# Performance work log

Hardware: AMD Instinct MI355X
Metric: run time of the kernel (lower is better)

## Reference

```python
import jax, jax.numpy as jnp
import numpy as np

DMODEL = 1024
DHIDDEN = 1024
N_HEAD = 16
HEAD_DIM = DHIDDEN // N_HEAD
B, S = 4, 2048


def setup_inputs() -> dict:
    key = jax.random.key(0)
    ks = jax.random.split(key, 10)
    sc = 1.0 / np.sqrt(DMODEL)
    return {
        "x": jax.random.normal(ks[0], (B, S, DMODEL), dtype=jnp.float32),
        "Wq": jax.random.normal(ks[1], (DMODEL, DHIDDEN), dtype=jnp.float32) * sc,
        "bq": jnp.zeros((DHIDDEN,), dtype=jnp.float32),
        "Wk": jax.random.normal(ks[2], (DMODEL, DHIDDEN), dtype=jnp.float32) * sc,
        "bk": jnp.zeros((DHIDDEN,), dtype=jnp.float32),
        "Wv": jax.random.normal(ks[3], (DMODEL, DHIDDEN), dtype=jnp.float32) * sc,
        "bv": jnp.zeros((DHIDDEN,), dtype=jnp.float32),
        "Wo": jax.random.normal(ks[4], (DHIDDEN, DMODEL), dtype=jnp.float32) * sc,
        "bo": jnp.zeros((DMODEL,), dtype=jnp.float32),
        "ln_gamma": jnp.ones((DMODEL,), dtype=jnp.float32),
        "ln_beta": jnp.zeros((DMODEL,), dtype=jnp.float32),
    }


def _layernorm(x, gamma, beta, eps=1e-5):
    mu = jnp.mean(x, axis=-1, keepdims=True)
    var = jnp.var(x, axis=-1, keepdims=True)
    return (x - mu) * jax.lax.rsqrt(var + eps) * gamma + beta


def reference(x, Wq, bq, Wk, bk, Wv, bv, Wo, bo, ln_gamma, ln_beta):
    b, s, _ = x.shape
    h = _layernorm(x, ln_gamma, ln_beta)           # [B,S,D]
    q = h @ Wq + bq                                 # [B,S,Dh]
    k = h @ Wk + bk
    v = h @ Wv + bv
    # [B,H,S,hd]
    q = q.reshape(b, s, N_HEAD, HEAD_DIM).transpose(0, 2, 1, 3)
    k = k.reshape(b, s, N_HEAD, HEAD_DIM).transpose(0, 2, 1, 3)
    v = v.reshape(b, s, N_HEAD, HEAD_DIM).transpose(0, 2, 1, 3)
    scores = jnp.einsum("bhqd,bhkd->bhqk", q, k) / np.sqrt(HEAD_DIM)
    causal = jnp.tril(jnp.ones((s, s), dtype=bool))  # [S,S]
    scores = jnp.where(causal, scores, jnp.finfo(scores.dtype).min)
    attn = jax.nn.softmax(scores, axis=-1)           # [B,H,S,S]
    out = jnp.einsum("bhqk,bhkd->bhqd", attn, v)     # [B,H,S,hd]
    out = out.transpose(0, 2, 1, 3).reshape(b, s, DHIDDEN)
    return out @ Wo + bo
```

## Files before the change

### kernel.cpp

```cpp
#include <hip/hip_runtime.h>


typedef short short8 __attribute__((ext_vector_type(8)));
typedef float floatx4 __attribute__((ext_vector_type(4)));
typedef unsigned short ushort4v __attribute__((ext_vector_type(4)));
typedef unsigned int uint2v __attribute__((ext_vector_type(2)));

#define MFMA16(a, b, c) __builtin_amdgcn_mfma_f32_16x16x32_bf16((a), (b), (c), 0, 0, 0)

__device__ __forceinline__ unsigned short f2bf(float f) {
  unsigned int u = __float_as_uint(f);
  u += 0x7FFFu + ((u >> 16) & 1u);
  return (unsigned short)(u >> 16);
}

#if defined(__has_builtin)
#if __has_builtin(__builtin_amdgcn_cvt_pk_bf16_f32)
#define HAVE_PK_BF16 1
#endif
#endif

__device__ __forceinline__ unsigned int pk_bf16(float a, float b) {
#ifdef HAVE_PK_BF16
  typedef __bf16 bf16x2_t __attribute__((ext_vector_type(2)));
  union { bf16x2_t v; unsigned int u; } cvt;
  cvt.v = __builtin_amdgcn_cvt_pk_bf16_f32(a, b);
  return cvt.u;
#else
  return (unsigned int)f2bf(a) | ((unsigned int)f2bf(b) << 16);
#endif
}

__device__ __forceinline__ void async_lds16(const void* g, void* l) {
  __builtin_amdgcn_global_load_lds(
      (const __attribute__((address_space(1))) void*)g,
      (__attribute__((address_space(3))) void*)l, 16, 0, 0);
}

__global__ __launch_bounds__(256) void transpose_w(
    const float* __restrict__ wq, const float* __restrict__ wk,
    const float* __restrict__ wv, const float* __restrict__ wo,
    unsigned short* __restrict__ wqkvT, unsigned short* __restrict__ woT) {
  __shared__ float t[64][65];
  const int r = threadIdx.x >> 6, c = threadIdx.x & 63;
  const int n0 = blockIdx.x * 64, k0 = blockIdx.y * 64, mz = blockIdx.z;
  const float* src = (mz == 0) ? wq : (mz == 1) ? wk : (mz == 2) ? wv : wo;
  unsigned short* dst = (mz == 3) ? woT : (wqkvT + (size_t)mz * 1024 * 1024);
#pragma unroll
  for (int i = r; i < 64; i += 4) t[i][c] = src[(size_t)(k0 + i) * 1024 + n0 + c];
  __syncthreads();
#pragma unroll
  for (int i = r; i < 64; i += 4) dst[(size_t)(n0 + i) * 1024 + k0 + c] = f2bf(t[c][i]);
}

__global__ __launch_bounds__(256) void ln_kernel(
    const float* __restrict__ x, const float* __restrict__ gamma,
    const float* __restrict__ beta, unsigned short* __restrict__ h) {
  const int row = blockIdx.x, tid = threadIdx.x;
  const float4 xv = ((const float4*)(x + (size_t)row * 1024))[tid];
  float s = xv.x + xv.y + xv.z + xv.w;
  float q = xv.x * xv.x + xv.y * xv.y + xv.z * xv.z + xv.w * xv.w;
#pragma unroll
  for (int off = 32; off > 0; off >>= 1) {
    s += __shfl_xor(s, off, 64);
    q += __shfl_xor(q, off, 64);
  }
  __shared__ float sm[4], qm[4];
  const int wave = tid >> 6, lane = tid & 63;
  if (lane == 0) { sm[wave] = s; qm[wave] = q; }
  __syncthreads();
  s = sm[0] + sm[1] + sm[2] + sm[3];
  q = qm[0] + qm[1] + qm[2] + qm[3];
  const float mean = s * (1.0f / 1024.0f);
  const float var = q * (1.0f / 1024.0f) - mean * mean;
  const float rstd = rsqrtf(var + 1e-5f);
  const float4 g = ((const float4*)gamma)[tid];
  const float4 bb = ((const float4*)beta)[tid];
  ushort4v o;
  o.x = f2bf((xv.x - mean) * rstd * g.x + bb.x);
  o.y = f2bf((xv.y - mean) * rstd * g.y + bb.y);
  o.z = f2bf((xv.z - mean) * rstd * g.z + bb.z);
  o.w = f2bf((xv.w - mean) * rstd * g.w + bb.w);
  ((ushort4v*)(h + (size_t)row * 1024))[tid] = o;
}

#define GEMM128_MAIN(A_, Bt_)                                                   \
  __shared__ __align__(16) unsigned short lA[128 * 32];                         \
  __shared__ __align__(16) unsigned short lB[128 * 32];                         \
  const int tid = threadIdx.x;                                                  \
  const int wave = tid >> 6, lane = tid & 63, quad = lane >> 4, l15 = lane & 15;\
  const int wm = wave >> 1, wn = wave & 1;                                      \
  const int m0 = blockIdx.x * 128, n0 = blockIdx.y * 128;                       \
  const int srow = tid >> 2, schunk = tid & 3;                                  \
  floatx4 acc[4][4];                                                            \
  _Pragma("unroll") for (int i = 0; i < 4; i++)                                 \
  _Pragma("unroll") for (int j = 0; j < 4; j++)                                 \
      acc[i][j] = (floatx4){0.f, 0.f, 0.f, 0.f};                                \
  for (int kt = 0; kt < 32; kt++) {                                             \
    const int k0 = kt * 32;                                                     \
    __syncthreads();                                                            \
    _Pragma("unroll") for (int j = 0; j < 2; j++) {                             \
      async_lds16(A_ + (size_t)(m0 + j * 64 + srow) * 1024 + k0 + schunk * 8,   \
                  (char*)lA + j * 4096 + wave * 1024);                          \
      async_lds16(Bt_ + (size_t)(n0 + j * 64 + srow) * 1024 + k0 + schunk * 8,  \
                  (char*)lB + j * 4096 + wave * 1024);                          \
    }                                                                           \
    __syncthreads();                                                            \
    short8 af[4], bf[4];                                                        \
    _Pragma("unroll") for (int i = 0; i < 4; i++) {                             \
      af[i] = *(const short8*)(lA + (wm * 64 + i * 16 + l15) * 32 + quad * 8);  \
      bf[i] = *(const short8*)(lB + (wn * 64 + i * 16 + l15) * 32 + quad * 8);  \
    }                                                                           \
    _Pragma("unroll") for (int mt = 0; mt < 4; mt++)                            \
    _Pragma("unroll") for (int nt = 0; nt < 4; nt++)                            \
        acc[mt][nt] = MFMA16(af[mt], bf[nt], acc[mt][nt]);                      \
  }

__global__ __launch_bounds__(256) void gemm_qkv(
    const unsigned short* __restrict__ A, const unsigned short* __restrict__ Bt,
    const float* __restrict__ bq, const float* __restrict__ bk,
    const float* __restrict__ bv, unsigned short* __restrict__ qo,
    unsigned short* __restrict__ ko, unsigned short* __restrict__ vT) {
  GEMM128_MAIN(A, Bt)
  const int sel = n0 >> 10;
  const float* bias = (sel == 0) ? bq : (sel == 1) ? bk : bv;
  const float oscale = (sel == 0) ? 0.18033688011112042f : 1.0f;
#pragma unroll
  for (int nt = 0; nt < 4; nt++) {
    const int n = n0 + wn * 64 + nt * 16 + l15;
    const int nn = n & 1023;
    const float bia = bias[nn];
    const int hidx = nn >> 6, d = nn & 63;
#pragma unroll
    for (int mt = 0; mt < 4; mt++) {
      const int mb = m0 + wm * 64 + mt * 16 + quad * 4;
      const int b = mb >> 11, sdx = mb & 2047;
      if (sel == 2) {
        ushort4v pk;
#pragma unroll
        for (int r = 0; r < 4; r++) pk[r] = f2bf(acc[mt][nt][r] + bia);
        *(ushort4v*)(vT + ((size_t)(b * 16 + hidx) * 64 + d) * 2048 + sdx) = pk;
      } else {
        unsigned short* dst =
            ((sel == 0) ? qo : ko) + ((size_t)(b * 16 + hidx) * 2048 + sdx) * 64 + d;
#pragma unroll
        for (int r = 0; r < 4; r++)
          dst[(size_t)r * 64] = f2bf((acc[mt][nt][r] + bia) * oscale);
      }
    }
  }
}

__global__ __launch_bounds__(256) void gemm_out(
    const unsigned short* __restrict__ A, const unsigned short* __restrict__ Bt,
    const float* __restrict__ bo, float* __restrict__ out) {
  GEMM128_MAIN(A, Bt)
#pragma unroll
  for (int nt = 0; nt < 4; nt++) {
    const int n = n0 + wn * 64 + nt * 16 + l15;
    const float bia = bo[n];
#pragma unroll
    for (int mt = 0; mt < 4; mt++) {
      const int m = m0 + wm * 64 + mt * 16 + quad * 4;
#pragma unroll
      for (int r = 0; r < 4; r++) out[(size_t)(m + r) * 1024 + n] = acc[mt][nt][r] + bia;
    }
  }
}

__global__ __launch_bounds__(256) void attn_kernel(
    const unsigned short* __restrict__ q, const unsigned short* __restrict__ k,
    const unsigned short* __restrict__ vT, unsigned short* __restrict__ ao) {
  __shared__ __align__(16) unsigned short lK[2][64 * 64];
  __shared__ __align__(16) unsigned short lV[2][64 * 64];
  __shared__ __align__(16) unsigned short lP[4][16 * 64];
  const int tid = threadIdx.x;
  const int wave = tid >> 6, lane = tid & 63, quad = lane >> 4, l15 = lane & 15;
  const int id = (int)blockIdx.x;
  const int bh = (id & 7) * 8 + ((id >> 3) & 7);
  const int qx = id >> 6;
  const int b = bh >> 4, hh = bh & 15;

  const unsigned short* qb = q + (size_t)bh * 2048 * 64;
  const unsigned short* kb = k + (size_t)bh * 2048 * 64;
  const unsigned short* vb = vT + (size_t)bh * 64 * 2048;
  unsigned short* pw = &lP[wave][0];

  const int srow = tid >> 3, schunk = tid & 7;

  const short8 ones8 = {0x3F80, 0x3F80, 0x3F80, 0x3F80,
                        0x3F80, 0x3F80, 0x3F80, 0x3F80};

  const int sw = l15 & 7;
  const int ph0 = (0 * 4 + quad) ^ sw, ph1 = (1 * 4 + quad) ^ sw;

#define STAGE_TILE(src_, rstride_, cbase_, dst_)                                 \
  _Pragma("unroll") for (int j = 0; j < 2; j++) {                                \
    const int row_ = j * 32 + srow;                                              \
    const int gch_ = schunk ^ (row_ & 7);                                        \
    async_lds16(src_ + (size_t)row_ * (rstride_) + (cbase_) + gch_ * 8,          \
                (char*)(dst_) + j * 4096 + wave * 1024);                         \
  }

#pragma unroll 1
  for (int pass = 0; pass < 2; pass++) {
    const int qt = pass ? qx : 31 - qx;
    const int q0w = qt * 64 + wave * 16;
    const int ntiles = qt + 1;

    short8 qf[2];
#pragma unroll
    for (int hf = 0; hf < 2; hf++)
      qf[hf] = *(const short8*)(qb + (size_t)(q0w + l15) * 64 + hf * 32 + quad * 8);

    floatx4 o[4];
#pragma unroll
    for (int nt = 0; nt < 4; nt++) o[nt] = (floatx4){0.f, 0.f, 0.f, 0.f};
    floatx4 lacc = {0.f, 0.f, 0.f, 0.f};

    __syncthreads();
    STAGE_TILE(kb, 64, 0, &lK[0][0])
    STAGE_TILE(vb, 2048, 0, &lV[0][0])
    int kbase = 0;
    for (int t = 0; t < ntiles; t++, kbase += 64) {
      __syncthreads();
      if (t + 1 < ntiles) {
        const int nb = (t + 1) & 1;
        STAGE_TILE(kb, 64, (size_t)(kbase + 64) * 64, &lK[nb][0])
        STAGE_TILE(vb, 2048, kbase + 64, &lV[nb][0])
      }
      const unsigned short* lKc = &lK[t & 1][0];
      const unsigned short* lVc = &lV[t & 1][0];

      floatx4 sc[4];
#pragma unroll
      for (int nt = 0; nt < 4; nt++) {
        sc[nt] = (floatx4){0.f, 0.f, 0.f, 0.f};
        {
          const short8 kf0 = *(const short8*)(lKc + (nt * 16 + l15) * 64 + ph0 * 8);
          sc[nt] = MFMA16(kf0, qf[0], sc[nt]);
          const short8 kf1 = *(const short8*)(lKc + (nt * 16 + l15) * 64 + ph1 * 8);
          sc[nt] = MFMA16(kf1, qf[1], sc[nt]);
        }
      }

      const bool needmask = (kbase + 63 > q0w);
      const int qg = q0w + l15;
#pragma unroll
      for (int nt = 0; nt < 4; nt++) {
        float p0 = exp2f(sc[nt][0]), p1 = exp2f(sc[nt][1]);
        float p2 = exp2f(sc[nt][2]), p3 = exp2f(sc[nt][3]);
        if (needmask) {
          const int kk = kbase + nt * 16 + quad * 4;
          if (kk + 0 > qg) p0 = 0.f;
          if (kk + 1 > qg) p1 = 0.f;
          if (kk + 2 > qg) p2 = 0.f;
          if (kk + 3 > qg) p3 = 0.f;
        }
        uint2v pk2;
        pk2.x = pk_bf16(p0, p1);
        pk2.y = pk_bf16(p2, p3);
        const int phys = (nt * 2 + (quad >> 1)) ^ sw;
        *(uint2v*)(pw + l15 * 64 + phys * 8 + (quad & 1) * 4) = pk2;
      }

      asm volatile("s_waitcnt lgkmcnt(0)" ::: "memory");

#pragma unroll
      for (int hf = 0; hf < 2; hf++) {
        const int ph = hf ? ph1 : ph0;
        const short8 pf = *(const short8*)(pw + l15 * 64 + ph * 8);
        lacc = MFMA16(ones8, pf, lacc);
#pragma unroll
        for (int nt = 0; nt < 4; nt++) {
          const short8 vf = *(const short8*)(lVc + (nt * 16 + l15) * 64 + ph * 8);
          o[nt] = MFMA16(vf, pf, o[nt]);
        }
      }
    }

    const float linv = 1.0f / lacc[0];
    unsigned short* dst = ao + ((size_t)b * 2048 + q0w + l15) * 1024 + hh * 64;
#pragma unroll
    for (int nt = 0; nt < 4; nt++) {
      uint2v pk2;
      pk2.x = pk_bf16(o[nt][0] * linv, o[nt][1] * linv);
      pk2.y = pk_bf16(o[nt][2] * linv, o[nt][3] * linv);
      *(uint2v*)(dst + nt * 16 + quad * 4) = pk2;
    }
  }
#undef STAGE_TILE
}

extern "C" void kernel_launch(void* const* d_in, const int* in_sizes, int n_in,
                              void* d_out, int out_size, void* d_ws, size_t ws_size,
                              hipStream_t stream) {
  const float* x = (const float*)d_in[0];
  const float* Wq = (const float*)d_in[1];
  const float* bq = (const float*)d_in[2];
  const float* Wk = (const float*)d_in[3];
  const float* bk = (const float*)d_in[4];
  const float* Wv = (const float*)d_in[5];
  const float* bv = (const float*)d_in[6];
  const float* Wo = (const float*)d_in[7];
  const float* bo = (const float*)d_in[8];
  const float* gamma = (const float*)d_in[9];
  const float* beta = (const float*)d_in[10];
  float* out = (float*)d_out;

  char* ws = (char*)d_ws;
  unsigned short* wqkvT = (unsigned short*)(ws + 0);
  unsigned short* woT   = (unsigned short*)(ws + 6291456);
  unsigned short* h     = (unsigned short*)(ws + 8388608);
  unsigned short* qb    = (unsigned short*)(ws + 25165824);
  unsigned short* kb    = (unsigned short*)(ws + 41943040);
  unsigned short* vT    = (unsigned short*)(ws + 58720256);
  unsigned short* ao    = (unsigned short*)(ws + 75497472);

  hipLaunchKernelGGL(transpose_w, dim3(16, 16, 4), dim3(256), 0, stream,
                     Wq, Wk, Wv, Wo, wqkvT, woT);
  hipLaunchKernelGGL(ln_kernel, dim3(8192), dim3(256), 0, stream, x, gamma, beta, h);
  hipLaunchKernelGGL(gemm_qkv, dim3(64, 24), dim3(256), 0, stream,
                     h, wqkvT, bq, bk, bv, qb, kb, vT);
  hipLaunchKernelGGL(attn_kernel, dim3(1024), dim3(256), 0, stream, qb, kb, vT, ao);
  hipLaunchKernelGGL(gemm_out, dim3(64, 8), dim3(256), 0, stream, ao, woT, bo, out);
}
```

Measured before the change: 288.7 us.

## Remap GEMM blocks per XCD and load attention V fragments directly from global

Both GEMMs now use a 1D grid whose block index is remapped so that the blocks on each XCD share the same column tiles of the weight matrix, aiming for better per-XCD L2 reuse. In the attention kernel, V tiles are no longer staged through LDS with double buffering. Each lane loads its V MFMA fragments straight from global memory into registers at the start of each tile, which removes the V LDS traffic and frees shared memory. The risk is that these global V loads are no longer overlapped via the async LDS pipeline, which may expose latency and raise register pressure.

```diff
diff --git a/kernel.cpp b/kernel.cpp
--- a/kernel.cpp
+++ b/kernel.cpp
@@ -84,13 +84,13 @@
   ((ushort4v*)(h + (size_t)row * 1024))[tid] = o;
 }
 
-#define GEMM128_MAIN(A_, Bt_)                                                   \
+#define GEMM128_MAIN(A_, Bt_, m0_, n0_)                                         \
   __shared__ __align__(16) unsigned short lA[128 * 32];                         \
   __shared__ __align__(16) unsigned short lB[128 * 32];                         \
   const int tid = threadIdx.x;                                                  \
   const int wave = tid >> 6, lane = tid & 63, quad = lane >> 4, l15 = lane & 15;\
   const int wm = wave >> 1, wn = wave & 1;                                      \
-  const int m0 = blockIdx.x * 128, n0 = blockIdx.y * 128;                       \
+  const int m0 = (m0_), n0 = (n0_);                                             \
   const int srow = tid >> 2, schunk = tid & 3;                                  \
   floatx4 acc[4][4];                                                            \
   _Pragma("unroll") for (int i = 0; i < 4; i++)                                 \
@@ -121,7 +121,9 @@
     const float* __restrict__ bq, const float* __restrict__ bk,
     const float* __restrict__ bv, unsigned short* __restrict__ qo,
     unsigned short* __restrict__ ko, unsigned short* __restrict__ vT) {
-  GEMM128_MAIN(A, Bt)
+  const int id = (int)blockIdx.x;
+  const int xcd = id & 7, rr = id >> 3;
+  GEMM128_MAIN(A, Bt, (rr / 3) * 128, (xcd * 3 + (rr % 3)) * 128)
   const int sel = n0 >> 10;
   const float* bias = (sel == 0) ? bq : (sel == 1) ? bk : bv;
   const float oscale = (sel == 0) ? 0.18033688011112042f : 1.0f;
@@ -154,7 +156,8 @@
 __global__ __launch_bounds__(256) void gemm_out(
     const unsigned short* __restrict__ A, const unsigned short* __restrict__ Bt,
     const float* __restrict__ bo, float* __restrict__ out) {
-  GEMM128_MAIN(A, Bt)
+  const int id = (int)blockIdx.x;
+  GEMM128_MAIN(A, Bt, (id >> 3) * 128, (id & 7) * 128)
 #pragma unroll
   for (int nt = 0; nt < 4; nt++) {
     const int n = n0 + wn * 64 + nt * 16 + l15;
@@ -172,7 +175,6 @@
     const unsigned short* __restrict__ q, const unsigned short* __restrict__ k,
     const unsigned short* __restrict__ vT, unsigned short* __restrict__ ao) {
   __shared__ __align__(16) unsigned short lK[2][64 * 64];
-  __shared__ __align__(16) unsigned short lV[2][64 * 64];
   __shared__ __align__(16) unsigned short lP[4][16 * 64];
   const int tid = threadIdx.x;
   const int wave = tid >> 6, lane = tid & 63, quad = lane >> 4, l15 = lane & 15;
@@ -194,12 +196,12 @@
   const int sw = l15 & 7;
   const int ph0 = (0 * 4 + quad) ^ sw, ph1 = (1 * 4 + quad) ^ sw;
 
-#define STAGE_TILE(src_, rstride_, cbase_, dst_)                                 \
+#define STAGE_K(kbase_, buf_)                                                    \
   _Pragma("unroll") for (int j = 0; j < 2; j++) {                                \
     const int row_ = j * 32 + srow;                                              \
     const int gch_ = schunk ^ (row_ & 7);                                        \
-    async_lds16(src_ + (size_t)row_ * (rstride_) + (cbase_) + gch_ * 8,          \
-                (char*)(dst_) + j * 4096 + wave * 1024);                         \
+    async_lds16(kb + (size_t)((kbase_) + row_) * 64 + (size_t)gch_ * 8,          \
+                (char*)&lK[buf_][0] + j * 4096 + wave * 1024);                   \
   }
 
 #pragma unroll 1
@@ -219,18 +221,21 @@
     floatx4 lacc = {0.f, 0.f, 0.f, 0.f};
 
     __syncthreads();
-    STAGE_TILE(kb, 64, 0, &lK[0][0])
-    STAGE_TILE(vb, 2048, 0, &lV[0][0])
+    STAGE_K(0, 0)
     int kbase = 0;
     for (int t = 0; t < ntiles; t++, kbase += 64) {
       __syncthreads();
-      if (t + 1 < ntiles) {
-        const int nb = (t + 1) & 1;
-        STAGE_TILE(kb, 64, (size_t)(kbase + 64) * 64, &lK[nb][0])
-        STAGE_TILE(vb, 2048, kbase + 64, &lV[nb][0])
-      }
+
+      short8 vf[4][2];
+#pragma unroll
+      for (int nt = 0; nt < 4; nt++)
+#pragma unroll
+        for (int hf = 0; hf < 2; hf++)
+          vf[nt][hf] = *(const short8*)(vb + (size_t)(nt * 16 + l15) * 2048 + kbase +
+                                        hf * 32 + quad * 8);
+
+      if (t + 1 < ntiles) { STAGE_K(kbase + 64, (t + 1) & 1) }
       const unsigned short* lKc = &lK[t & 1][0];
-      const unsigned short* lVc = &lV[t & 1][0];
 
       floatx4 sc[4];
 #pragma unroll
@@ -272,10 +277,7 @@
         const short8 pf = *(const short8*)(pw + l15 * 64 + ph * 8);
         lacc = MFMA16(ones8, pf, lacc);
 #pragma unroll
-        for (int nt = 0; nt < 4; nt++) {
-          const short8 vf = *(const short8*)(lVc + (nt * 16 + l15) * 64 + ph * 8);
-          o[nt] = MFMA16(vf, pf, o[nt]);
-        }
+        for (int nt = 0; nt < 4; nt++) o[nt] = MFMA16(vf[nt][hf], pf, o[nt]);
       }
     }
 
@@ -289,7 +291,7 @@
       *(uint2v*)(dst + nt * 16 + quad * 4) = pk2;
     }
   }
-#undef STAGE_TILE
+#undef STAGE_K
 }
 
 extern "C" void kernel_launch(void* const* d_in, const int* in_sizes, int n_in,
@@ -320,8 +322,8 @@
   hipLaunchKernelGGL(transpose_w, dim3(16, 16, 4), dim3(256), 0, stream,
                      Wq, Wk, Wv, Wo, wqkvT, woT);
   hipLaunchKernelGGL(ln_kernel, dim3(8192), dim3(256), 0, stream, x, gamma, beta, h);
-  hipLaunchKernelGGL(gemm_qkv, dim3(64, 24), dim3(256), 0, stream,
+  hipLaunchKernelGGL(gemm_qkv, dim3(1536), dim3(256), 0, stream,
                      h, wqkvT, bq, bk, bv, qb, kb, vT);
   hipLaunchKernelGGL(attn_kernel, dim3(1024), dim3(256), 0, stream, qb, kb, vT, ao);
-  hipLaunchKernelGGL(gemm_out, dim3(64, 8), dim3(256), 0, stream, ao, woT, bo, out);
-}
+  hipLaunchKernelGGL(gemm_out, dim3(512), dim3(256), 0, stream, ao, woT, bo, out);
+}
```

Measured after the change: 379.4 us. 31.4% more time.

## Fuse attention's two query-tile passes into one K/V sweep and remap GEMM blocks per XCD

Applied to the files above, without the earlier changes.

The attention kernel used to make two sequential passes (query tile 31-qx, then qx), each streaming K/V separately. It now processes both query tiles in one loop over the longer tile's K/V range, sharing each staged K/V tile and its LDS fragment loads across both. It also requests 4 blocks per CU via launch bounds. The QKV and output GEMMs switch to a 1D grid with a block-id remap so each XCD works on a contiguous group of weight columns, aiming for better L2 reuse. The cost is higher register pressure from doubled accumulators, and extra branching on the dual flag.

```diff
diff --git a/kernel.cpp b/kernel.cpp
--- a/kernel.cpp
+++ b/kernel.cpp
@@ -84,13 +84,13 @@
   ((ushort4v*)(h + (size_t)row * 1024))[tid] = o;
 }
 
-#define GEMM128_MAIN(A_, Bt_)                                                   \
+#define GEMM128_MAIN(A_, Bt_, m0_, n0_)                                         \
   __shared__ __align__(16) unsigned short lA[128 * 32];                         \
   __shared__ __align__(16) unsigned short lB[128 * 32];                         \
   const int tid = threadIdx.x;                                                  \
   const int wave = tid >> 6, lane = tid & 63, quad = lane >> 4, l15 = lane & 15;\
   const int wm = wave >> 1, wn = wave & 1;                                      \
-  const int m0 = blockIdx.x * 128, n0 = blockIdx.y * 128;                       \
+  const int m0 = (m0_), n0 = (n0_);                                             \
   const int srow = tid >> 2, schunk = tid & 3;                                  \
   floatx4 acc[4][4];                                                            \
   _Pragma("unroll") for (int i = 0; i < 4; i++)                                 \
@@ -121,7 +121,9 @@
     const float* __restrict__ bq, const float* __restrict__ bk,
     const float* __restrict__ bv, unsigned short* __restrict__ qo,
     unsigned short* __restrict__ ko, unsigned short* __restrict__ vT) {
-  GEMM128_MAIN(A, Bt)
+  const int id = (int)blockIdx.x;
+  const int xcd = id & 7, rr = id >> 3;
+  GEMM128_MAIN(A, Bt, (rr / 3) * 128, (xcd * 3 + (rr % 3)) * 128)
   const int sel = n0 >> 10;
   const float* bias = (sel == 0) ? bq : (sel == 1) ? bk : bv;
   const float oscale = (sel == 0) ? 0.18033688011112042f : 1.0f;
@@ -154,7 +156,8 @@
 __global__ __launch_bounds__(256) void gemm_out(
     const unsigned short* __restrict__ A, const unsigned short* __restrict__ Bt,
     const float* __restrict__ bo, float* __restrict__ out) {
-  GEMM128_MAIN(A, Bt)
+  const int id = (int)blockIdx.x;
+  GEMM128_MAIN(A, Bt, (id >> 3) * 128, (id & 7) * 128)
 #pragma unroll
   for (int nt = 0; nt < 4; nt++) {
     const int n = n0 + wn * 64 + nt * 16 + l15;
@@ -168,7 +171,7 @@
   }
 }
 
-__global__ __launch_bounds__(256) void attn_kernel(
+__global__ __launch_bounds__(256, 4) void attn_kernel(
     const unsigned short* __restrict__ q, const unsigned short* __restrict__ k,
     const unsigned short* __restrict__ vT, unsigned short* __restrict__ ao) {
   __shared__ __align__(16) unsigned short lK[2][64 * 64];
@@ -180,6 +183,9 @@
   const int bh = (id & 7) * 8 + ((id >> 3) & 7);
   const int qx = id >> 6;
   const int b = bh >> 4, hh = bh & 15;
+  const int qtA = 31 - qx, qtB = qx;
+  const int q0wA = qtA * 64 + wave * 16, q0wB = qtB * 64 + wave * 16;
+  const int ntiles = qtA + 1;
 
   const unsigned short* qb = q + (size_t)bh * 2048 * 64;
   const unsigned short* kb = k + (size_t)bh * 2048 * 64;
@@ -202,54 +208,57 @@
                 (char*)(dst_) + j * 4096 + wave * 1024);                         \
   }
 
-#pragma unroll 1
-  for (int pass = 0; pass < 2; pass++) {
-    const int qt = pass ? qx : 31 - qx;
-    const int q0w = qt * 64 + wave * 16;
-    const int ntiles = qt + 1;
-
-    short8 qf[2];
-#pragma unroll
-    for (int hf = 0; hf < 2; hf++)
-      qf[hf] = *(const short8*)(qb + (size_t)(q0w + l15) * 64 + hf * 32 + quad * 8);
-
-    floatx4 o[4];
-#pragma unroll
-    for (int nt = 0; nt < 4; nt++) o[nt] = (floatx4){0.f, 0.f, 0.f, 0.f};
-    floatx4 lacc = {0.f, 0.f, 0.f, 0.f};
-
+  short8 qfA[2], qfB[2];
+#pragma unroll
+  for (int hf = 0; hf < 2; hf++) {
+    qfA[hf] = *(const short8*)(qb + (size_t)(q0wA + l15) * 64 + hf * 32 + quad * 8);
+    qfB[hf] = *(const short8*)(qb + (size_t)(q0wB + l15) * 64 + hf * 32 + quad * 8);
+  }
+
+  floatx4 oA[4], oB[4];
+#pragma unroll
+  for (int nt = 0; nt < 4; nt++) {
+    oA[nt] = (floatx4){0.f, 0.f, 0.f, 0.f};
+    oB[nt] = (floatx4){0.f, 0.f, 0.f, 0.f};
+  }
+  floatx4 laccA = {0.f, 0.f, 0.f, 0.f}, laccB = {0.f, 0.f, 0.f, 0.f};
+
+  STAGE_TILE(kb, 64, 0, &lK[0][0])
+  STAGE_TILE(vb, 2048, 0, &lV[0][0])
+  int kbase = 0;
+  for (int t = 0; t < ntiles; t++, kbase += 64) {
     __syncthreads();
-    STAGE_TILE(kb, 64, 0, &lK[0][0])
-    STAGE_TILE(vb, 2048, 0, &lV[0][0])
-    int kbase = 0;
-    for (int t = 0; t < ntiles; t++, kbase += 64) {
-      __syncthreads();
-      if (t + 1 < ntiles) {
-        const int nb = (t + 1) & 1;
-        STAGE_TILE(kb, 64, (size_t)(kbase + 64) * 64, &lK[nb][0])
-        STAGE_TILE(vb, 2048, kbase + 64, &lV[nb][0])
-      }
-      const unsigned short* lKc = &lK[t & 1][0];
-      const unsigned short* lVc = &lV[t & 1][0];
-
-      floatx4 sc[4];
+    if (t + 1 < ntiles) {
+      const int nb = (t + 1) & 1;
+      STAGE_TILE(kb, 64, (size_t)(kbase + 64) * 64, &lK[nb][0])
+      STAGE_TILE(vb, 2048, (size_t)(kbase + 64), &lV[nb][0])
+    }
+    const unsigned short* lKc = &lK[t & 1][0];
+    const unsigned short* lVc = &lV[t & 1][0];
+    const bool dual = (t <= qtB);
+
+    floatx4 scA[4], scB[4];
+#pragma unroll
+    for (int nt = 0; nt < 4; nt++) {
+      scA[nt] = (floatx4){0.f, 0.f, 0.f, 0.f};
+      scB[nt] = (floatx4){0.f, 0.f, 0.f, 0.f};
+      const short8 kf0 = *(const short8*)(lKc + (nt * 16 + l15) * 64 + ph0 * 8);
+      const short8 kf1 = *(const short8*)(lKc + (nt * 16 + l15) * 64 + ph1 * 8);
+      scA[nt] = MFMA16(kf0, qfA[0], scA[nt]);
+      scA[nt] = MFMA16(kf1, qfA[1], scA[nt]);
+      if (dual) {
+        scB[nt] = MFMA16(kf0, qfB[0], scB[nt]);
+        scB[nt] = MFMA16(kf1, qfB[1], scB[nt]);
+      }
+    }
+
+    {
+      const bool needmask = (kbase + 63 > q0wA);
+      const int qg = q0wA + l15;
 #pragma unroll
       for (int nt = 0; nt < 4; nt++) {
-        sc[nt] = (floatx4){0.f, 0.f, 0.f, 0.f};
-        {
-          const short8 kf0 = *(const short8*)(lKc + (nt * 16 + l15) * 64 + ph0 * 8);
-          sc[nt] = MFMA16(kf0, qf[0], sc[nt]);
-          const short8 kf1 = *(const short8*)(lKc + (nt * 16 + l15) * 64 + ph1 * 8);
-          sc[nt] = MFMA16(kf1, qf[1], sc[nt]);
-        }
-      }
-
-      const bool needmask = (kbase + 63 > q0w);
-      const int qg = q0w + l15;
-#pragma unroll
-      for (int nt = 0; nt < 4; nt++) {
-        float p0 = exp2f(sc[nt][0]), p1 = exp2f(sc[nt][1]);
-        float p2 = exp2f(sc[nt][2]), p3 = exp2f(sc[nt][3]);
+        float p0 = exp2f(scA[nt][0]), p1 = exp2f(scA[nt][1]);
+        float p2 = exp2f(scA[nt][2]), p3 = exp2f(scA[nt][3]);
         if (needmask) {
           const int kk = kbase + nt * 16 + quad * 4;
           if (kk + 0 > qg) p0 = 0.f;
@@ -263,29 +272,71 @@
         const int phys = (nt * 2 + (quad >> 1)) ^ sw;
         *(uint2v*)(pw + l15 * 64 + phys * 8 + (quad & 1) * 4) = pk2;
       }
-
+    }
+    asm volatile("s_waitcnt lgkmcnt(0)" ::: "memory");
+    short8 pfA0 = *(const short8*)(pw + l15 * 64 + ph0 * 8);
+    short8 pfA1 = *(const short8*)(pw + l15 * 64 + ph1 * 8);
+
+    short8 pfB0, pfB1;
+    if (dual) {
+      const bool needmask = (kbase + 63 > q0wB);
+      const int qg = q0wB + l15;
+#pragma unroll
+      for (int nt = 0; nt < 4; nt++) {
+        float p0 = exp2f(scB[nt][0]), p1 = exp2f(scB[nt][1]);
+        float p2 = exp2f(scB[nt][2]), p3 = exp2f(scB[nt][3]);
+        if (needmask) {
+          const int kk = kbase + nt * 16 + quad * 4;
+          if (kk + 0 > qg) p0 = 0.f;
+          if (kk + 1 > qg) p1 = 0.f;
+          if (kk + 2 > qg) p2 = 0.f;
+          if (kk + 3 > qg) p3 = 0.f;
+        }
+        uint2v pk2;
+        pk2.x = pk_bf16(p0, p1);
+        pk2.y = pk_bf16(p2, p3);
+        const int phys = (nt * 2 + (quad >> 1)) ^ sw;
+        *(uint2v*)(pw + l15 * 64 + phys * 8 + (quad & 1) * 4) = pk2;
+      }
       asm volatile("s_waitcnt lgkmcnt(0)" ::: "memory");
-
-#pragma unroll
-      for (int hf = 0; hf < 2; hf++) {
-        const int ph = hf ? ph1 : ph0;
-        const short8 pf = *(const short8*)(pw + l15 * 64 + ph * 8);
-        lacc = MFMA16(ones8, pf, lacc);
-#pragma unroll
-        for (int nt = 0; nt < 4; nt++) {
-          const short8 vf = *(const short8*)(lVc + (nt * 16 + l15) * 64 + ph * 8);
-          o[nt] = MFMA16(vf, pf, o[nt]);
-        }
-      }
-    }
-
-    const float linv = 1.0f / lacc[0];
-    unsigned short* dst = ao + ((size_t)b * 2048 + q0w + l15) * 1024 + hh * 64;
+      pfB0 = *(const short8*)(pw + l15 * 64 + ph0 * 8);
+      pfB1 = *(const short8*)(pw + l15 * 64 + ph1 * 8);
+    }
+
+#pragma unroll
+    for (int hf = 0; hf < 2; hf++) {
+      const short8 pfA = hf ? pfA1 : pfA0;
+      laccA = MFMA16(ones8, pfA, laccA);
+      if (dual) laccB = MFMA16(ones8, hf ? pfB1 : pfB0, laccB);
+      const int ph = hf ? ph1 : ph0;
+#pragma unroll
+      for (int nt = 0; nt < 4; nt++) {
+        const short8 vf = *(const short8*)(lVc + (nt * 16 + l15) * 64 + ph * 8);
+        oA[nt] = MFMA16(vf, pfA, oA[nt]);
+        if (dual) oB[nt] = MFMA16(vf, hf ? pfB1 : pfB0, oB[nt]);
+      }
+    }
+  }
+
+  {
+    const float linv = 1.0f / laccA[0];
+    unsigned short* dst = ao + ((size_t)b * 2048 + q0wA + l15) * 1024 + hh * 64;
 #pragma unroll
     for (int nt = 0; nt < 4; nt++) {
       uint2v pk2;
-      pk2.x = pk_bf16(o[nt][0] * linv, o[nt][1] * linv);
-      pk2.y = pk_bf16(o[nt][2] * linv, o[nt][3] * linv);
+      pk2.x = pk_bf16(oA[nt][0] * linv, oA[nt][1] * linv);
+      pk2.y = pk_bf16(oA[nt][2] * linv, oA[nt][3] * linv);
+      *(uint2v*)(dst + nt * 16 + quad * 4) = pk2;
+    }
+  }
+  {
+    const float linv = 1.0f / laccB[0];
+    unsigned short* dst = ao + ((size_t)b * 2048 + q0wB + l15) * 1024 + hh * 64;
+#pragma unroll
+    for (int nt = 0; nt < 4; nt++) {
+      uint2v pk2;
+      pk2.x = pk_bf16(oB[nt][0] * linv, oB[nt][1] * linv);
+      pk2.y = pk_bf16(oB[nt][2] * linv, oB[nt][3] * linv);
       *(uint2v*)(dst + nt * 16 + quad * 4) = pk2;
     }
   }
@@ -320,8 +371,8 @@
   hipLaunchKernelGGL(transpose_w, dim3(16, 16, 4), dim3(256), 0, stream,
                      Wq, Wk, Wv, Wo, wqkvT, woT);
   hipLaunchKernelGGL(ln_kernel, dim3(8192), dim3(256), 0, stream, x, gamma, beta, h);
-  hipLaunchKernelGGL(gemm_qkv, dim3(64, 24), dim3(256), 0, stream,
+  hipLaunchKernelGGL(gemm_qkv, dim3(1536), dim3(256), 0, stream,
                      h, wqkvT, bq, bk, bv, qb, kb, vT);
   hipLaunchKernelGGL(attn_kernel, dim3(1024), dim3(256), 0, stream, qb, kb, vT, ao);
-  hipLaunchKernelGGL(gemm_out, dim3(64, 8), dim3(256), 0, stream, ao, woT, bo, out);
-}
+  hipLaunchKernelGGL(gemm_out, dim3(512), dim3(256), 0, stream, ao, woT, bo, out);
+}
```

Result: slower. 298.9 us (+3.5%).
